# Kernel optimization log

Hardware: AMD Instinct MI355X
Metric: run time of the kernel (lower is better)

Reference implementation:

```python
import jax, jax.numpy as jnp
import numpy as np

# Protocol constants (config.protocol); standard DCE-MRI values.
TR = 0.005                       # repetition time [s]
ALPHA = 15.0 / 180.0 * np.pi     # flip angle [rad]
DELTT = 4.0 / 60.0               # temporal resolution [min]
R1_RELAX = 4.5                   # contrast agent relaxivity [/mM/s]
N_TIME = 112
BATCH = 262144


def setup_inputs() -> dict:
    key = jax.random.key(0)
    k1, k2, k3, k4, k5 = jax.random.split(key, 5)
    # Physiologically plausible positive ranges (avoid division blowups).
    ktrans = jax.random.uniform(k1, (BATCH, 1), jnp.float32, 0.01, 1.0)
    vp = jax.random.uniform(k2, (BATCH, 1), jnp.float32, 0.0, 0.1)
    ve = jax.random.uniform(k3, (BATCH, 1), jnp.float32, 0.05, 1.0)
    T10 = jax.random.uniform(k4, (BATCH, 1), jnp.float32, 0.5, 2.0)
    CAp = jax.random.uniform(k5, (BATCH, N_TIME), jnp.float32, 0.0, 1.0)
    return {"ktrans": ktrans, "vp": vp, "ve": ve, "T10": T10, "CAp": CAp}


def _cae(CAp, ktrans, ve):
    # Original: Toeplitz matrix ce_x with ce[b,i] = ktrans*deltt *
    #   sum_{j<=i} CAp[b,j] * exp(-ktrans/ve * (i-j) * deltt)
    # == first-order IIR recurrence c_i = decay * c_{i-1} + CAp[:, i].
    decay = jnp.exp(-ktrans / ve * DELTT)[:, 0]  # [B]

    def step(c, cap_t):
        c = c * decay + cap_t
        return c, c

    c0 = jnp.zeros(CAp.shape[0], CAp.dtype)
    _, cs = jax.lax.scan(step, c0, CAp.T)  # cs: [N, B]
    return (ktrans * DELTT) * cs.T          # [B, N]


def reference(ktrans, vp, ve, T10, CAp):
    ce = _cae(CAp, ktrans, ve)                 # [B, N]
    ct = vp * CAp + ce                         # tissue concentration
    R1t = 1.0 / T10 + R1_RELAX * ct            # [B, N]
    e = jnp.exp(-TR * R1t)
    s = (1.0 - e) * np.sin(ALPHA) / (1.0 - e * np.cos(ALPHA))
    return s * 20.0


if __name__ == "__main__":
    out = reference(**setup_inputs())
    print(out.shape, out.dtype)
```

## Files before the change

kernel.cpp:

```cpp
#include <hip/hip_runtime.h>

#define N_TIME  112
#define BATCH   262144
#define NF4ROW  28
#define NCH     7

__device__ __forceinline__ float sig(float cap, float c, float vp,
                                     float kd, float invT10) {
    const float TR     = 0.005f;
    const float R1     = 4.5f;
    const float SINA20 = 20.0f * 0.25881904510252074f;
    const float COSA   = 0.96592582628906829f;
    float ct = vp * cap + kd * c;
    float e  = __expf(-TR * (invT10 + R1 * ct));
    return (1.0f - e) * SINA20 * __builtin_amdgcn_rcpf(1.0f - e * COSA);
}

__global__ __launch_bounds__(256) void etofts_kernel(
    const float* __restrict__ ktrans_p,
    const float* __restrict__ vp_p,
    const float* __restrict__ ve_p,
    const float* __restrict__ T10_p,
    const float* __restrict__ cap_p,
    float* __restrict__ out_p)
{
    const int tid = blockIdx.x * blockDim.x + threadIdx.x;
    const int row = tid >> 2;
    const int t   = tid & 3;

    const float DELTT  = 4.0f / 60.0f;
    const float ktrans = ktrans_p[row];
    const float vp     = vp_p[row];
    const float ve     = ve_p[row];
    const float invT10 = __builtin_amdgcn_rcpf(T10_p[row]);
    const float kd     = ktrans * DELTT;

    const float d1  = __expf(-ktrans / ve * DELTT);
    const float d2  = d1 * d1;
    const float d3  = d2 * d1;
    const float d4  = d2 * d2;
    const float d8  = d4 * d4;
    const float d12 = d8 * d4;
    const float d16 = d8 * d8;
    const float dt4 = (t == 0) ? 1.0f : (t == 1) ? d4 : (t == 2) ? d8 : d12;

    const float4* capv = reinterpret_cast<const float4*>(cap_p) + (size_t)row * NF4ROW + t;
    float4*       outv = reinterpret_cast<float4*>(out_p)       + (size_t)row * NF4ROW + t;

    float c_in = 0.0f;

    float4 xa = capv[0];
    float4 xb = capv[4];

    #pragma unroll
    for (int ch = 0; ch < NCH; ++ch) {
        float4 xf;
        if (ch + 2 < NCH) xf = capv[(ch + 2) * 4];

        const float4 x = xa;

        float s0 = x.x;
        float s1 = fmaf(d1, s0, x.y);
        float s2 = fmaf(d1, s1, x.z);
        float s3 = fmaf(d1, s2, x.w);

        float S  = s3;
        float v1 = __shfl_up(S, 1, 4);
        if (t >= 1) S = fmaf(d4, v1, S);
        float v2 = __shfl_up(S, 2, 4);
        if (t >= 2) S = fmaf(d8, v2, S);

        float E   = __shfl_up(S, 1, 4);
        float tin = (t == 0) ? dt4 * c_in : fmaf(dt4, c_in, E);

        float S3 = __shfl(S, 3, 4);
        c_in = fmaf(d16, c_in, S3);

        float c0 = fmaf(d1, tin, s0);
        float c1 = fmaf(d2, tin, s1);
        float c2 = fmaf(d3, tin, s2);
        float c3 = fmaf(d4, tin, s3);

        float4 y;
        y.x = sig(x.x, c0, vp, kd, invT10);
        y.y = sig(x.y, c1, vp, kd, invT10);
        y.z = sig(x.z, c2, vp, kd, invT10);
        y.w = sig(x.w, c3, vp, kd, invT10);
        outv[ch * 4] = y;

        xa = xb;
        xb = xf;
    }
}

extern "C" void kernel_launch(void* const* d_in, const int* in_sizes, int n_in,
                              void* d_out, int out_size, void* d_ws, size_t ws_size,
                              hipStream_t stream) {
    const float* ktrans = (const float*)d_in[0];
    const float* vp     = (const float*)d_in[1];
    const float* ve     = (const float*)d_in[2];
    const float* T10    = (const float*)d_in[3];
    const float* CAp    = (const float*)d_in[4];
    float* out = (float*)d_out;

    dim3 block(256);
    dim3 grid((BATCH * 4) / 256);
    etofts_kernel<<<grid, block, 0, stream>>>(ktrans, vp, ve, T10, CAp, out);
}
```

Measured before the change: 43.80 us.

## Load all row chunks upfront and split scan into local, carry, and output phases

Issues all seven float4 loads for a thread's row slice at the start instead of using a two-deep prefetch. The per-chunk local scan and cross-lane shuffles are computed independently of the carry, then the short carry chain runs separately, and the output pass applies the carries. This is meant to expose more memory-level parallelism and ILP by taking the serial carry off the shuffle/load critical path, at the cost of more live registers per thread.

```diff
diff --git a/kernel.cpp b/kernel.cpp
--- a/kernel.cpp
+++ b/kernel.cpp
@@ -47,49 +47,49 @@
     const float4* capv = reinterpret_cast<const float4*>(cap_p) + (size_t)row * NF4ROW + t;
     float4*       outv = reinterpret_cast<float4*>(out_p)       + (size_t)row * NF4ROW + t;
 
-    float c_in = 0.0f;
+    float4 x[NCH];
+    #pragma unroll
+    for (int ch = 0; ch < NCH; ++ch) x[ch] = capv[ch * 4];
 
-    float4 xa = capv[0];
-    float4 xb = capv[4];
-
+    float s1[NCH], s2[NCH], s3[NCH], E[NCH], T[NCH];
     #pragma unroll
     for (int ch = 0; ch < NCH; ++ch) {
-        float4 xf;
-        if (ch + 2 < NCH) xf = capv[(ch + 2) * 4];
+        float a0 = x[ch].x;
+        float a1 = fmaf(d1, a0, x[ch].y);
+        float a2 = fmaf(d1, a1, x[ch].z);
+        float a3 = fmaf(d1, a2, x[ch].w);
+        s1[ch] = a1; s2[ch] = a2; s3[ch] = a3;
 
-        const float4 x = xa;
-
-        float s0 = x.x;
-        float s1 = fmaf(d1, s0, x.y);
-        float s2 = fmaf(d1, s1, x.z);
-        float s3 = fmaf(d1, s2, x.w);
-
-        float S  = s3;
+        float S  = a3;
         float v1 = __shfl_up(S, 1, 4);
         if (t >= 1) S = fmaf(d4, v1, S);
         float v2 = __shfl_up(S, 2, 4);
         if (t >= 2) S = fmaf(d8, v2, S);
 
-        float E   = __shfl_up(S, 1, 4);
-        float tin = (t == 0) ? dt4 * c_in : fmaf(dt4, c_in, E);
+        E[ch] = __shfl_up(S, 1, 4);
+        T[ch] = __shfl(S, 3, 4);
+    }
 
-        float S3 = __shfl(S, 3, 4);
-        c_in = fmaf(d16, c_in, S3);
+    float C[NCH];
+    C[0] = 0.0f;
+    #pragma unroll
+    for (int ch = 0; ch < NCH - 1; ++ch) C[ch + 1] = fmaf(d16, C[ch], T[ch]);
 
-        float c0 = fmaf(d1, tin, s0);
-        float c1 = fmaf(d2, tin, s1);
-        float c2 = fmaf(d3, tin, s2);
-        float c3 = fmaf(d4, tin, s3);
+    #pragma unroll
+    for (int ch = 0; ch < NCH; ++ch) {
+        float tin = (t == 0) ? dt4 * C[ch] : fmaf(dt4, C[ch], E[ch]);
+
+        float c0 = fmaf(d1, tin, x[ch].x);
+        float c1 = fmaf(d2, tin, s1[ch]);
+        float c2 = fmaf(d3, tin, s2[ch]);
+        float c3 = fmaf(d4, tin, s3[ch]);
 
         float4 y;
-        y.x = sig(x.x, c0, vp, kd, invT10);
-        y.y = sig(x.y, c1, vp, kd, invT10);
-        y.z = sig(x.z, c2, vp, kd, invT10);
-        y.w = sig(x.w, c3, vp, kd, invT10);
+        y.x = sig(x[ch].x, c0, vp, kd, invT10);
+        y.y = sig(x[ch].y, c1, vp, kd, invT10);
+        y.z = sig(x[ch].z, c2, vp, kd, invT10);
+        y.w = sig(x[ch].w, c3, vp, kd, invT10);
         outv[ch * 4] = y;
-
-        xa = xb;
-        xb = xf;
     }
 }
 
```

New measurement: 43.88 us. Within noise of the previous version (+0.2%).
